# Kernel optimization log

Hardware: AMD Instinct MI355X
Metric: run time of the kernel (lower is better)

The kernel has to match this reference:

```python
import jax, jax.numpy as jnp
import numpy as np

B, T, F, H = 16, 512, 32, 128
EPS = 1e-5


def _layer_norm(y, g, b):
    mu = jnp.mean(y, axis=-1, keepdims=True)
    var = jnp.mean(jnp.square(y - mu), axis=-1, keepdims=True)
    return (y - mu) * jax.lax.rsqrt(var + EPS) * g + b


def setup_inputs() -> dict:
    key = jax.random.key(0)
    ks = jax.random.split(key, 16)
    s = 0.1  # small param scale
    return {
        "x": jax.random.normal(ks[0], (B, T, F), jnp.float32),
        # weight GRN (input_size == hidden == F, skip is Identity)
        "wg_fc1_w": jax.random.normal(ks[1], (F, F), jnp.float32) * s,
        "wg_fc1_b": jnp.zeros((F,), jnp.float32),
        "wg_fc2_w": jax.random.normal(ks[2], (2 * F, F), jnp.float32) * s,
        "wg_fc2_b": jnp.zeros((2 * F,), jnp.float32),
        "wg_ln_g": jnp.ones((F,), jnp.float32),
        "wg_ln_b": jnp.zeros((F,), jnp.float32),
        # per-feature GRNs (input_size=1 -> hidden H), batched over F
        "f_fc1_w": jax.random.normal(ks[3], (F, H), jnp.float32) * s,   # torch Linear(1,H).weight squeezed
        "f_fc1_b": jax.random.normal(ks[4], (F, H), jnp.float32) * s,
        "f_fc2_w": jax.random.normal(ks[5], (F, 2 * H, H), jnp.float32) * s,
        "f_fc2_b": jax.random.normal(ks[6], (F, 2 * H), jnp.float32) * s,
        "f_skip_w": jax.random.normal(ks[7], (F, H), jnp.float32) * s,  # Linear(1,H).weight squeezed
        "f_skip_b": jax.random.normal(ks[8], (F, H), jnp.float32) * s,
        "f_ln_g": jnp.ones((F, H), jnp.float32),
        "f_ln_b": jnp.zeros((F, H), jnp.float32),
    }


def reference(x, wg_fc1_w, wg_fc1_b, wg_fc2_w, wg_fc2_b, wg_ln_g, wg_ln_b,
              f_fc1_w, f_fc1_b, f_fc2_w, f_fc2_b, f_skip_w, f_skip_b,
              f_ln_g, f_ln_b):
    # --- weight GRN over the feature axis: [B,T,F] -> [B,T,F] ---
    h = jax.nn.elu(jnp.einsum('btf,gf->btg', x, wg_fc1_w) + wg_fc1_b)
    h2 = jnp.einsum('btg,kg->btk', h, wg_fc2_w) + wg_fc2_b  # [B,T,2F]
    a, g = jnp.split(h2, 2, axis=-1)
    glu = a * jax.nn.sigmoid(g)
    weights = jax.nn.softmax(_layer_norm(x + glu, wg_ln_g, wg_ln_b), axis=-1)  # [B,T,F]

    # --- all F per-feature GRNs batched (input width 1) ---
    xe = x[..., None]                                   # [B,T,F,1]
    h = jax.nn.elu(xe * f_fc1_w + f_fc1_b)              # [B,T,F,H]
    h2 = jnp.einsum('btfh,fgh->btfg', h, f_fc2_w) + f_fc2_b  # [B,T,F,2H]
    a, g = jnp.split(h2, 2, axis=-1)
    glu = a * jax.nn.sigmoid(g)                         # [B,T,F,H]
    res = xe * f_skip_w + f_skip_b                      # [B,T,F,H]
    y = _layer_norm(res + glu, f_ln_g, f_ln_b)          # per-feature LN params [F,H]

    # --- softmax-weighted combine ---
    return jnp.einsum('btf,btfh->bth', weights, y)      # [B,T,H]
```

## Files before the change

kernel.cpp:

```cpp
#include <hip/hip_runtime.h>
#include <cstdint>
#include <cstddef>

#define EPS 1e-5f

typedef float    f4     __attribute__((ext_vector_type(4)));
typedef float    f2     __attribute__((ext_vector_type(2)));
typedef _Float16 half8  __attribute__((ext_vector_type(8)));
typedef _Float16 half4  __attribute__((ext_vector_type(4)));
typedef _Float16 half2v __attribute__((ext_vector_type(2)));

#define S_HV 136
#define S_XS 33
#define S_OUT 132
#define F_BLK 8

__global__ __launch_bounds__(256) void k_conv(const float* __restrict__ in,
                                              _Float16* __restrict__ out) {
    int i = (blockIdx.x * 256 + threadIdx.x) * 4;
    f4 v = *(const f4*)(in + i);
    half4 h;
    h[0] = (_Float16)v[0]; h[1] = (_Float16)v[1];
    h[2] = (_Float16)v[2]; h[3] = (_Float16)v[3];
    *(half4*)(out + i) = h;
}

__global__ __launch_bounds__(256) void k_weights(
    const float* __restrict__ x, const float* __restrict__ w1,
    const float* __restrict__ b1, const float* __restrict__ w2,
    const float* __restrict__ b2, const float* __restrict__ lng,
    const float* __restrict__ lnb, float* __restrict__ wts) {
    __shared__ float w1s[32 * S_XS];
    __shared__ float w2s[64 * S_XS];
    __shared__ float xsW[32 * S_XS];

    const int tid = threadIdx.x;
    const int lane = tid & 63;
    const int f = lane & 31;
    const int wv = tid >> 6;
    const int row0 = blockIdx.x * 32;

    for (int i = tid; i < 1024; i += 256) {
        int r = i >> 5, c = i & 31;
        w1s[r * S_XS + c] = w1[i];
        xsW[r * S_XS + c] = x[(size_t)row0 * 32 + i];
    }
    for (int i = tid; i < 2048; i += 256) {
        int r = i >> 5, c = i & 31;
        w2s[r * S_XS + c] = w2[i];
    }
    const float b1f = b1[f], b2a = b2[f], b2g = b2[f + 32];
    const float lgf = lng[f], lbf = lnb[f];
    __syncthreads();

    for (int rr = 0; rr < 8; ++rr) {
        const int r = wv * 8 + rr;
        float acc = b1f;
        #pragma unroll
        for (int k = 0; k < 32; ++k)
            acc = fmaf(w1s[f * S_XS + k], xsW[r * S_XS + k], acc);
        float hval = acc > 0.f ? acc : __expf(acc) - 1.f;

        float a = b2a, g = b2g;
        #pragma unroll
        for (int k = 0; k < 32; ++k) {
            float hk = __shfl(hval, k, 64);
            a = fmaf(w2s[f * S_XS + k], hk, a);
            g = fmaf(w2s[(f + 32) * S_XS + k], hk, g);
        }
        float xv = xsW[r * S_XS + f];
        float v = xv + a * (1.f / (1.f + __expf(-g)));

        float s = v;
        #pragma unroll
        for (int o = 1; o < 64; o <<= 1) s += __shfl_xor(s, o, 64);
        float mu = s * (1.f / 64.f);
        float d = v - mu;
        float sq = d * d;
        #pragma unroll
        for (int o = 1; o < 64; o <<= 1) sq += __shfl_xor(sq, o, 64);
        float y = d * rsqrtf(sq * (1.f / 64.f) + EPS) * lgf + lbf;

        float m = y;
        #pragma unroll
        for (int o = 1; o < 64; o <<= 1) m = fmaxf(m, __shfl_xor(m, o, 64));
        float e = __expf(y - m);
        float se = e;
        #pragma unroll
        for (int o = 1; o < 64; o <<= 1) se += __shfl_xor(se, o, 64);
        if (lane < 32) wts[(size_t)(row0 + r) * 32 + f] = e * 2.f / se;
    }
}

__global__ __launch_bounds__(256, 4) void k_main(
    const float* __restrict__ x,
    const _Float16* __restrict__ w2h,
    const float* __restrict__ fc1w,
    const float* __restrict__ fc1b,
    const float* __restrict__ fc2b,
    const float* __restrict__ skw,
    const float* __restrict__ skb,
    const float* __restrict__ lng,
    const float* __restrict__ lnb,
    const float* __restrict__ wts,
    float* __restrict__ out)
{
    __shared__ __align__(16) _Float16 hvs[2 * 32 * S_HV];
    __shared__ float xs[32 * S_XS];
    __shared__ float wss[32 * S_XS];
    __shared__ f2 part[2 * 32 * 5];
    float* outs = (float*)hvs;

    const int tid = threadIdx.x;
    const int tile = blockIdx.x >> 2;
    const int fbase = (blockIdx.x & 3) * F_BLK;
    const int row0 = tile * 32;

    for (int i = tid; i < 1024; i += 256) {
        int r = i >> 5, c = i & 31;
        xs[r * S_XS + c] = x[(size_t)row0 * 32 + i];
        wss[r * S_XS + c] = wts[(size_t)row0 * 32 + i];
    }

    const int lane = tid & 63;
    const int wv = tid >> 6;
    const int l15 = lane & 15;
    const int q = lane >> 4;
    const int ga0 = wv * 32;
    const int h0 = lane * 2;
    const int rb = wv * 8;

    float out_acc[2][2][4];
    #pragma unroll
    for (int mt = 0; mt < 2; ++mt)
        #pragma unroll
        for (int n = 0; n < 2; ++n)
            #pragma unroll
            for (int rg = 0; rg < 4; ++rg) out_acc[mt][n][rg] = 0.f;

    auto compute_hv = [&](int f, _Float16* hb) {
        f2 w1v = *(const f2*)(fc1w + f * 128 + h0);
        f2 b1v = *(const f2*)(fc1b + f * 128 + h0);
        #pragma unroll
        for (int rr = 0; rr < 8; ++rr) {
            int r = rb + rr;
            float xv = xs[r * S_XS + f];
            float t0 = fmaf(xv, w1v[0], b1v[0]);
            float t1 = fmaf(xv, w1v[1], b1v[1]);
            t0 = t0 > 0.f ? t0 : __expf(t0) - 1.f;
            t1 = t1 > 0.f ? t1 : __expf(t1) - 1.f;
            half2v pk; pk[0] = (_Float16)t0; pk[1] = (_Float16)t1;
            *(half2v*)&hb[r * S_HV + h0] = pk;
        }
    };

    __syncthreads();
    compute_hv(fbase, hvs);
    __syncthreads();

    int p = 0;
    for (int fi = 0; fi < F_BLK; ++fi) {
        const int f = fbase + fi;
        const _Float16* hb = hvs + p * (32 * S_HV);

        f4 acc[4][2];
        {
            f4 z; z[0] = 0.f; z[1] = 0.f; z[2] = 0.f; z[3] = 0.f;
            #pragma unroll
            for (int mt = 0; mt < 4; ++mt) { acc[mt][0] = z; acc[mt][1] = z; }
        }
        const _Float16* wb = w2h + ((size_t)f * 256 + l15) * 128 + 8 * q;
        #pragma unroll
        for (int kq = 0; kq < 4; ++kq) {
            const int k0 = kq * 32;
            half8 b0 = *(const half8*)&hb[l15 * S_HV + k0 + 8 * q];
            half8 b1 = *(const half8*)&hb[(16 + l15) * S_HV + k0 + 8 * q];
            #pragma unroll
            for (int mt = 0; mt < 4; ++mt) {
                const int gb = ga0 + (mt & 1) * 16 + (mt >> 1) * 128;
                half8 a = *(const half8*)(wb + (size_t)gb * 128 + k0);
                acc[mt][0] = __builtin_amdgcn_mfma_f32_16x16x32_f16(a, b0, acc[mt][0], 0, 0, 0);
                acc[mt][1] = __builtin_amdgcn_mfma_f32_16x16x32_f16(a, b1, acc[mt][1], 0, 0, 0);
            }
        }

        float vv[2][2][4];
        float sn[2] = {0.f, 0.f}, sqn[2] = {0.f, 0.f};
        float xvn[2];
        xvn[0] = xs[l15 * S_XS + f];
        xvn[1] = xs[(16 + l15) * S_XS + f];
        #pragma unroll
        for (int mt = 0; mt < 2; ++mt) {
            #pragma unroll
            for (int rg = 0; rg < 4; ++rg) {
                const int h = ga0 + 16 * mt + 4 * q + rg;
                float ba = fc2b[f * 256 + h];
                float bg = fc2b[f * 256 + 128 + h];
                float sw = skw[f * 128 + h];
                float sb = skb[f * 128 + h];
                #pragma unroll
                for (int n = 0; n < 2; ++n) {
                    float a = acc[mt][n][rg] + ba;
                    float g = acc[mt + 2][n][rg] + bg;
                    float sig = 1.f / (1.f + __expf(-g));
                    float val = fmaf(xvn[n], sw, sb) + a * sig;
                    vv[mt][n][rg] = val;
                    sn[n] += val;
                    sqn[n] = fmaf(val, val, sqn[n]);
                }
            }
        }
        #pragma unroll
        for (int o = 16; o < 64; o <<= 1) {
            #pragma unroll
            for (int n = 0; n < 2; ++n) {
                sn[n] += __shfl_xor(sn[n], o, 64);
                sqn[n] += __shfl_xor(sqn[n], o, 64);
            }
        }
        if (q == 0) {
            #pragma unroll
            for (int n = 0; n < 2; ++n) {
                f2 pr; pr[0] = sn[n]; pr[1] = sqn[n];
                part[p * 160 + (n * 16 + l15) * 5 + wv] = pr;
            }
        }

        if (fi + 1 < F_BLK) compute_hv(f + 1, hvs + (1 - p) * (32 * S_HV));
        __syncthreads();

        float mu_[2], wr_[2], wl_[2];
        #pragma unroll
        for (int n = 0; n < 2; ++n) {
            const int c = n * 16 + l15;
            f2 t0 = part[p * 160 + c * 5 + 0];
            f2 t1 = part[p * 160 + c * 5 + 1];
            f2 t2 = part[p * 160 + c * 5 + 2];
            f2 t3 = part[p * 160 + c * 5 + 3];
            float ss = (t0[0] + t1[0]) + (t2[0] + t3[0]);
            float qv = (t0[1] + t1[1]) + (t2[1] + t3[1]);
            float mu = ss * (1.f / 128.f);
            float var = qv * (1.f / 128.f) - mu * mu;
            float rstd = rsqrtf(fmaxf(var, 0.f) + EPS);
            float wrow = wss[c * S_XS + f];
            mu_[n] = mu; wr_[n] = wrow * rstd; wl_[n] = wrow;
        }
        #pragma unroll
        for (int mt = 0; mt < 2; ++mt) {
            #pragma unroll
            for (int rg = 0; rg < 4; ++rg) {
                const int h = ga0 + 16 * mt + 4 * q + rg;
                float lg = lng[f * 128 + h];
                float lb = lnb[f * 128 + h];
                #pragma unroll
                for (int n = 0; n < 2; ++n) {
                    float u = (vv[mt][n][rg] - mu_[n]) * wr_[n];
                    out_acc[mt][n][rg] = fmaf(u, lg, fmaf(wl_[n], lb, out_acc[mt][n][rg]));
                }
            }
        }
        p ^= 1;
    }

    __syncthreads();
    #pragma unroll
    for (int mt = 0; mt < 2; ++mt)
        #pragma unroll
        for (int n = 0; n < 2; ++n)
            #pragma unroll
            for (int rg = 0; rg < 4; ++rg)
                outs[(n * 16 + l15) * S_OUT + ga0 + 16 * mt + 4 * q + rg] =
                    out_acc[mt][n][rg];
    __syncthreads();
    const int oh = tid & 127;
    const int r0b = (tid >> 7) * 16;
    #pragma unroll
    for (int rr = 0; rr < 16; ++rr) {
        int r = r0b + rr;
        atomicAdd(&out[(size_t)(row0 + r) * 128 + oh], outs[r * S_OUT + oh]);
    }
}

extern "C" void kernel_launch(void* const* d_in, const int* in_sizes, int n_in,
                              void* d_out, int out_size, void* d_ws, size_t ws_size,
                              hipStream_t stream) {
    const float* x     = (const float*)d_in[0];
    const float* wg1w  = (const float*)d_in[1];
    const float* wg1b  = (const float*)d_in[2];
    const float* wg2w  = (const float*)d_in[3];
    const float* wg2b  = (const float*)d_in[4];
    const float* wglng = (const float*)d_in[5];
    const float* wglnb = (const float*)d_in[6];
    const float* fc1w  = (const float*)d_in[7];
    const float* fc1b  = (const float*)d_in[8];
    const float* fc2w  = (const float*)d_in[9];
    const float* fc2b  = (const float*)d_in[10];
    const float* skw   = (const float*)d_in[11];
    const float* skb   = (const float*)d_in[12];
    const float* lng   = (const float*)d_in[13];
    const float* lnb   = (const float*)d_in[14];
    float* out = (float*)d_out;

    _Float16* w2h = (_Float16*)d_ws;
    float* wts = (float*)((char*)d_ws + (2u << 20));

    k_conv<<<dim3(1024), dim3(256), 0, stream>>>(fc2w, w2h);
    k_weights<<<dim3(256), dim3(256), 0, stream>>>(x, wg1w, wg1b, wg2w, wg2b,
                                                   wglng, wglnb, wts);
    hipMemsetAsync(out, 0, (size_t)out_size * sizeof(float), stream);
    k_main<<<dim3(1024), dim3(256), 0, stream>>>(x, w2h, fc1w, fc1b, fc2b,
                                                 skw, skb, lng, lnb, wts, out);
}
```

Baseline: 184.6 us.

## Compute ELU hidden directly in MFMA A-fragments, drop LDS staging and cross-wave LN

Each wave now owns 16 rows and all 256 output columns of the per-feature matmul. The ELU hidden activations are computed straight into register A-fragments, so the shared-memory hv double buffer, the cross-wave LayerNorm partial exchange and most barriers go away. The LN reduction becomes a within-wave shuffle, and the output is written with per-lane atomics without an LDS transpose. Tiles grow to 64 rows with 4 features per block, the weight B-fragments are prefetched from global one step ahead, and launch bounds drop to 3 blocks per CU. The price is more registers (16 accumulators and 32 output values per lane), lower occupancy, and uncoalesced atomics.

```diff
diff --git a/kernel.cpp b/kernel.cpp
--- a/kernel.cpp
+++ b/kernel.cpp
@@ -8,12 +8,9 @@
 typedef float    f2     __attribute__((ext_vector_type(2)));
 typedef _Float16 half8  __attribute__((ext_vector_type(8)));
 typedef _Float16 half4  __attribute__((ext_vector_type(4)));
-typedef _Float16 half2v __attribute__((ext_vector_type(2)));
-
-#define S_HV 136
+
 #define S_XS 33
-#define S_OUT 132
-#define F_BLK 8
+#define F_BLK 4
 
 __global__ __launch_bounds__(256) void k_conv(const float* __restrict__ in,
                                               _Float16* __restrict__ out) {
@@ -92,7 +89,7 @@
     }
 }
 
-__global__ __launch_bounds__(256, 4) void k_main(
+__global__ __launch_bounds__(256, 3) void k_main(
     const float* __restrict__ x,
     const _Float16* __restrict__ w2h,
     const float* __restrict__ fc1w,
@@ -105,18 +102,15 @@
     const float* __restrict__ wts,
     float* __restrict__ out)
 {
-    __shared__ __align__(16) _Float16 hvs[2 * 32 * S_HV];
-    __shared__ float xs[32 * S_XS];
-    __shared__ float wss[32 * S_XS];
-    __shared__ f2 part[2 * 32 * 5];
-    float* outs = (float*)hvs;
+    __shared__ float xs[64 * S_XS];
+    __shared__ float wss[64 * S_XS];
 
     const int tid = threadIdx.x;
-    const int tile = blockIdx.x >> 2;
-    const int fbase = (blockIdx.x & 3) * F_BLK;
-    const int row0 = tile * 32;
-
-    for (int i = tid; i < 1024; i += 256) {
+    const int tile = blockIdx.x >> 3;
+    const int fbase = (blockIdx.x & 7) * F_BLK;
+    const int row0 = tile * 64;
+
+    for (int i = tid; i < 2048; i += 256) {
         int r = i >> 5, c = i & 31;
         xs[r * S_XS + c] = x[(size_t)row0 * 32 + i];
         wss[r * S_XS + c] = wts[(size_t)row0 * 32 + i];
@@ -126,158 +120,129 @@
     const int wv = tid >> 6;
     const int l15 = lane & 15;
     const int q = lane >> 4;
-    const int ga0 = wv * 32;
-    const int h0 = lane * 2;
-    const int rb = wv * 8;
-
-    float out_acc[2][2][4];
+    const int rA = wv * 16 + l15;
+
+    float out_acc[8][4];
     #pragma unroll
-    for (int mt = 0; mt < 2; ++mt)
-        #pragma unroll
-        for (int n = 0; n < 2; ++n)
-            #pragma unroll
-            for (int rg = 0; rg < 4; ++rg) out_acc[mt][n][rg] = 0.f;
-
-    auto compute_hv = [&](int f, _Float16* hb) {
-        f2 w1v = *(const f2*)(fc1w + f * 128 + h0);
-        f2 b1v = *(const f2*)(fc1b + f * 128 + h0);
-        #pragma unroll
-        for (int rr = 0; rr < 8; ++rr) {
-            int r = rb + rr;
-            float xv = xs[r * S_XS + f];
-            float t0 = fmaf(xv, w1v[0], b1v[0]);
-            float t1 = fmaf(xv, w1v[1], b1v[1]);
-            t0 = t0 > 0.f ? t0 : __expf(t0) - 1.f;
-            t1 = t1 > 0.f ? t1 : __expf(t1) - 1.f;
-            half2v pk; pk[0] = (_Float16)t0; pk[1] = (_Float16)t1;
-            *(half2v*)&hb[r * S_HV + h0] = pk;
-        }
-    };
-
-    __syncthreads();
-    compute_hv(fbase, hvs);
-    __syncthreads();
-
-    int p = 0;
+    for (int nt = 0; nt < 8; ++nt)
+        #pragma unroll
+        for (int rg = 0; rg < 4; ++rg) out_acc[nt][rg] = 0.f;
+
     for (int fi = 0; fi < F_BLK; ++fi) {
         const int f = fbase + fi;
-        const _Float16* hb = hvs + p * (32 * S_HV);
-
-        f4 acc[4][2];
+        __syncthreads();
+
+        const float xvA = xs[rA * S_XS + f];
+        half8 A[4];
+        #pragma unroll
+        for (int kq = 0; kq < 4; ++kq) {
+            const float* wp = fc1w + f * 128 + kq * 32 + 8 * q;
+            const float* bp = fc1b + f * 128 + kq * 32 + 8 * q;
+            f4 w0 = *(const f4*)wp, w1v = *(const f4*)(wp + 4);
+            f4 b0 = *(const f4*)bp, b1v = *(const f4*)(bp + 4);
+            half8 a;
+            #pragma unroll
+            for (int j = 0; j < 4; ++j) {
+                float t = fmaf(xvA, w0[j], b0[j]);
+                t = t > 0.f ? t : __expf(t) - 1.f;
+                a[j] = (_Float16)t;
+            }
+            #pragma unroll
+            for (int j = 0; j < 4; ++j) {
+                float t = fmaf(xvA, w1v[j], b1v[j]);
+                t = t > 0.f ? t : __expf(t) - 1.f;
+                a[4 + j] = (_Float16)t;
+            }
+            A[kq] = a;
+        }
+
+        f4 acc[16];
         {
             f4 z; z[0] = 0.f; z[1] = 0.f; z[2] = 0.f; z[3] = 0.f;
             #pragma unroll
-            for (int mt = 0; mt < 4; ++mt) { acc[mt][0] = z; acc[mt][1] = z; }
-        }
-        const _Float16* wb = w2h + ((size_t)f * 256 + l15) * 128 + 8 * q;
-        #pragma unroll
-        for (int kq = 0; kq < 4; ++kq) {
-            const int k0 = kq * 32;
-            half8 b0 = *(const half8*)&hb[l15 * S_HV + k0 + 8 * q];
-            half8 b1 = *(const half8*)&hb[(16 + l15) * S_HV + k0 + 8 * q];
-            #pragma unroll
-            for (int mt = 0; mt < 4; ++mt) {
-                const int gb = ga0 + (mt & 1) * 16 + (mt >> 1) * 128;
-                half8 a = *(const half8*)(wb + (size_t)gb * 128 + k0);
-                acc[mt][0] = __builtin_amdgcn_mfma_f32_16x16x32_f16(a, b0, acc[mt][0], 0, 0, 0);
-                acc[mt][1] = __builtin_amdgcn_mfma_f32_16x16x32_f16(a, b1, acc[mt][1], 0, 0, 0);
-            }
-        }
-
-        float vv[2][2][4];
-        float sn[2] = {0.f, 0.f}, sqn[2] = {0.f, 0.f};
-        float xvn[2];
-        xvn[0] = xs[l15 * S_XS + f];
-        xvn[1] = xs[(16 + l15) * S_XS + f];
-        #pragma unroll
-        for (int mt = 0; mt < 2; ++mt) {
+            for (int nt = 0; nt < 16; ++nt) acc[nt] = z;
+        }
+        const _Float16* bbase = w2h + ((size_t)f * 256 + l15) * 128 + 8 * q;
+        half8 Bf[2][4];
+        #pragma unroll
+        for (int kq = 0; kq < 4; ++kq)
+            Bf[0][kq] = *(const half8*)(bbase + kq * 32);
+        #pragma unroll
+        for (int nt = 0; nt < 16; ++nt) {
+            const int cur = nt & 1;
+            if (nt < 15) {
+                const _Float16* bn = bbase + (nt + 1) * (16 * 128);
+                #pragma unroll
+                for (int kq = 0; kq < 4; ++kq)
+                    Bf[cur ^ 1][kq] = *(const half8*)(bn + kq * 32);
+            }
+            #pragma unroll
+            for (int kq = 0; kq < 4; ++kq)
+                acc[nt] = __builtin_amdgcn_mfma_f32_16x16x32_f16(
+                    A[kq], Bf[cur][kq], acc[nt], 0, 0, 0);
+        }
+
+        float xr[4], wrow[4];
+        #pragma unroll
+        for (int rg = 0; rg < 4; ++rg) {
+            xr[rg] = xs[(wv * 16 + 4 * q + rg) * S_XS + f];
+            wrow[rg] = wss[(wv * 16 + 4 * q + rg) * S_XS + f];
+        }
+        float vv[8][4];
+        float s[4] = {0.f, 0.f, 0.f, 0.f}, sq[4] = {0.f, 0.f, 0.f, 0.f};
+        #pragma unroll
+        for (int nt = 0; nt < 8; ++nt) {
+            const int h = nt * 16 + l15;
+            float ba = fc2b[f * 256 + h];
+            float bg = fc2b[f * 256 + 128 + h];
+            float sw = skw[f * 128 + h];
+            float sb = skb[f * 128 + h];
             #pragma unroll
             for (int rg = 0; rg < 4; ++rg) {
-                const int h = ga0 + 16 * mt + 4 * q + rg;
-                float ba = fc2b[f * 256 + h];
-                float bg = fc2b[f * 256 + 128 + h];
-                float sw = skw[f * 128 + h];
-                float sb = skb[f * 128 + h];
-                #pragma unroll
-                for (int n = 0; n < 2; ++n) {
-                    float a = acc[mt][n][rg] + ba;
-                    float g = acc[mt + 2][n][rg] + bg;
-                    float sig = 1.f / (1.f + __expf(-g));
-                    float val = fmaf(xvn[n], sw, sb) + a * sig;
-                    vv[mt][n][rg] = val;
-                    sn[n] += val;
-                    sqn[n] = fmaf(val, val, sqn[n]);
-                }
-            }
-        }
-        #pragma unroll
-        for (int o = 16; o < 64; o <<= 1) {
-            #pragma unroll
-            for (int n = 0; n < 2; ++n) {
-                sn[n] += __shfl_xor(sn[n], o, 64);
-                sqn[n] += __shfl_xor(sqn[n], o, 64);
-            }
-        }
-        if (q == 0) {
-            #pragma unroll
-            for (int n = 0; n < 2; ++n) {
-                f2 pr; pr[0] = sn[n]; pr[1] = sqn[n];
-                part[p * 160 + (n * 16 + l15) * 5 + wv] = pr;
-            }
-        }
-
-        if (fi + 1 < F_BLK) compute_hv(f + 1, hvs + (1 - p) * (32 * S_HV));
-        __syncthreads();
-
-        float mu_[2], wr_[2], wl_[2];
-        #pragma unroll
-        for (int n = 0; n < 2; ++n) {
-            const int c = n * 16 + l15;
-            f2 t0 = part[p * 160 + c * 5 + 0];
-            f2 t1 = part[p * 160 + c * 5 + 1];
-            f2 t2 = part[p * 160 + c * 5 + 2];
-            f2 t3 = part[p * 160 + c * 5 + 3];
-            float ss = (t0[0] + t1[0]) + (t2[0] + t3[0]);
-            float qv = (t0[1] + t1[1]) + (t2[1] + t3[1]);
-            float mu = ss * (1.f / 128.f);
-            float var = qv * (1.f / 128.f) - mu * mu;
-            float rstd = rsqrtf(fmaxf(var, 0.f) + EPS);
-            float wrow = wss[c * S_XS + f];
-            mu_[n] = mu; wr_[n] = wrow * rstd; wl_[n] = wrow;
-        }
-        #pragma unroll
-        for (int mt = 0; mt < 2; ++mt) {
+                float a = acc[nt][rg] + ba;
+                float g = acc[nt + 8][rg] + bg;
+                float sig = 1.f / (1.f + __expf(-g));
+                float val = fmaf(xr[rg], sw, sb) + a * sig;
+                vv[nt][rg] = val;
+                s[rg] += val;
+                sq[rg] = fmaf(val, val, sq[rg]);
+            }
+        }
+        #pragma unroll
+        for (int o = 1; o < 16; o <<= 1) {
             #pragma unroll
             for (int rg = 0; rg < 4; ++rg) {
-                const int h = ga0 + 16 * mt + 4 * q + rg;
-                float lg = lng[f * 128 + h];
-                float lb = lnb[f * 128 + h];
-                #pragma unroll
-                for (int n = 0; n < 2; ++n) {
-                    float u = (vv[mt][n][rg] - mu_[n]) * wr_[n];
-                    out_acc[mt][n][rg] = fmaf(u, lg, fmaf(wl_[n], lb, out_acc[mt][n][rg]));
-                }
-            }
-        }
-        p ^= 1;
-    }
-
-    __syncthreads();
+                s[rg] += __shfl_xor(s[rg], o, 64);
+                sq[rg] += __shfl_xor(sq[rg], o, 64);
+            }
+        }
+        float mu[4], wr[4];
+        #pragma unroll
+        for (int rg = 0; rg < 4; ++rg) {
+            mu[rg] = s[rg] * (1.f / 128.f);
+            float var = sq[rg] * (1.f / 128.f) - mu[rg] * mu[rg];
+            wr[rg] = wrow[rg] * rsqrtf(fmaxf(var, 0.f) + EPS);
+        }
+        #pragma unroll
+        for (int nt = 0; nt < 8; ++nt) {
+            const int h = nt * 16 + l15;
+            float lg = lng[f * 128 + h];
+            float lb = lnb[f * 128 + h];
+            #pragma unroll
+            for (int rg = 0; rg < 4; ++rg) {
+                float u = (vv[nt][rg] - mu[rg]) * wr[rg];
+                out_acc[nt][rg] = fmaf(u, lg, fmaf(wrow[rg], lb, out_acc[nt][rg]));
+            }
+        }
+    }
+
     #pragma unroll
-    for (int mt = 0; mt < 2; ++mt)
-        #pragma unroll
-        for (int n = 0; n < 2; ++n)
-            #pragma unroll
-            for (int rg = 0; rg < 4; ++rg)
-                outs[(n * 16 + l15) * S_OUT + ga0 + 16 * mt + 4 * q + rg] =
-                    out_acc[mt][n][rg];
-    __syncthreads();
-    const int oh = tid & 127;
-    const int r0b = (tid >> 7) * 16;
-    #pragma unroll
-    for (int rr = 0; rr < 16; ++rr) {
-        int r = r0b + rr;
-        atomicAdd(&out[(size_t)(row0 + r) * 128 + oh], outs[r * S_OUT + oh]);
+    for (int nt = 0; nt < 8; ++nt) {
+        #pragma unroll
+        for (int rg = 0; rg < 4; ++rg) {
+            const int r = row0 + wv * 16 + 4 * q + rg;
+            atomicAdd(&out[(size_t)r * 128 + nt * 16 + l15], out_acc[nt][rg]);
+        }
     }
 }
 
```

Result: slower. 274.7 us (+48.8%).
